# Kernel optimization log

Measured on AMD Instinct MI355X. Metric: run time of the kernel, lower is better.

Reference implementation:

```python
import jax, jax.numpy as jnp
import numpy as np

N_NODES = 59392        # batch_size * node_each_graph = 512 * 116
N_EDGES = 1187840      # avg degree 20

def _graph_conv(h, src, dst, W, b, out_norm, in_norm):
    # DGL GraphConv, norm='both': act((D_in^-1/2 A D_out^-1/2 h) W + b)
    h = h * out_norm[:, None]
    m = jax.ops.segment_sum(h[src], dst, num_segments=N_NODES)  # sparse aggregation
    m = m * in_norm[:, None]
    return jax.nn.relu(m @ W + b)

def setup_inputs() -> dict:
    key = jax.random.key(0)
    ks = jax.random.split(key, 8)
    feat = jax.random.normal(ks[0], (N_NODES, 116), dtype=jnp.float32)
    src = jax.random.randint(ks[1], (N_EDGES,), 0, N_NODES)
    dst = jax.random.randint(ks[2], (N_EDGES,), 0, N_NODES)
    W1 = jax.random.normal(ks[3], (116, 64), dtype=jnp.float32) * 0.05
    b1 = jnp.zeros((64,), dtype=jnp.float32)
    W2 = jax.random.normal(ks[4], (64, 64), dtype=jnp.float32) * 0.05
    b2 = jnp.zeros((64,), dtype=jnp.float32)
    Wc = jax.random.normal(ks[5], (116 * 64, 2), dtype=jnp.float32) * 0.05
    bc = jnp.zeros((2,), dtype=jnp.float32)
    return {"feat": feat, "src": src, "dst": dst, "batch_size": 512,
            "W1": W1, "b1": b1, "W2": W2, "b2": b2, "Wc": Wc, "bc": bc}

def reference(feat, src, dst, batch_size, W1, b1, W2, b2, Wc, bc):
    ones = jnp.ones((N_EDGES,), dtype=jnp.float32)
    out_deg = jax.ops.segment_sum(ones, src, num_segments=N_NODES)
    in_deg = jax.ops.segment_sum(ones, dst, num_segments=N_NODES)
    out_norm = jax.lax.rsqrt(jnp.maximum(out_deg, 1.0))
    in_norm = jax.lax.rsqrt(jnp.maximum(in_deg, 1.0))
    h = _graph_conv(feat, src, dst, W1, b1, out_norm, in_norm)
    # dropout is identity in eval mode
    h = _graph_conv(h, src, dst, W2, b2, out_norm, in_norm)
    h = h.reshape(batch_size, -1)  # (B, node_each_graph * hid)
    return h @ Wc + bc
```

## Files before the change

kernel.cpp:

```cpp
#include <hip/hip_runtime.h>

#define N_NODES 59392
#define N_EDGES 1187840
#define F_IN 116
#define F_HID 64
#define BATCH 512
#define NPG 116
#define CCAP 64
#define NSLD 80
#define EPSD (N_EDGES / NSLD)
#define NSLS 80
#define EPSS (N_EDGES / NSLS)
#define NBIN4 (N_NODES / 4)
#define GPB 4
#define NPB (NPG / GPB)
#define SCAN_BLK (N_NODES / 256)
#define GEMM_BLK 640

typedef __attribute__((ext_vector_type(8))) short short8;
typedef __attribute__((ext_vector_type(4))) float float4v;
typedef __attribute__((ext_vector_type(2))) float float2v;

__device__ __forceinline__ float u2f(unsigned u) {
    union { unsigned u; float f; } x; x.u = u; return x.f;
}
__device__ __forceinline__ float bf2f(unsigned short h) {
    union { unsigned u; float f; } x; x.u = (unsigned)h << 16; return x.f;
}
__device__ __forceinline__ unsigned short f2bf(float f) {
    union { float f; unsigned u; } x; x.f = f;
    unsigned r = x.u + 0x7FFF + ((x.u >> 16) & 1);
    return (unsigned short)(r >> 16);
}

__global__ __launch_bounds__(1024) void hist_kernel(const int* __restrict__ src,
                                                    const int* __restrict__ dst,
                                                    unsigned char* __restrict__ cnt2,
                                                    unsigned char* __restrict__ cnt2s) {
    __shared__ unsigned bins[NBIN4];
    int tid = threadIdx.x;
    int b = blockIdx.x;
    const int* __restrict__ idx;
    unsigned char* outp;
    int slice;
    if (b < NSLD) {
        slice = b; idx = dst; outp = cnt2;
    } else {
        slice = b - NSLD; idx = src; outp = cnt2s;
    }
    long ebase = (long)slice * EPSD;
    for (int k = tid; k < NBIN4; k += 1024) bins[k] = 0;
    __syncthreads();
    for (int k = tid; k < EPSD; k += 1024) {
        int v = idx[ebase + k];
        atomicAdd(&bins[v >> 2], 1u << ((v & 3) * 8));
    }
    __syncthreads();
    unsigned* op = (unsigned*)(outp + (size_t)slice * N_NODES);
    for (int k = tid; k < NBIN4; k += 1024) op[k] = bins[k];
}

__global__ __launch_bounds__(256) void scan_kernel(unsigned char* __restrict__ cnt2,
                                                   const unsigned char* __restrict__ cnt2s,
                                                   float* __restrict__ onorm,
                                                   float* __restrict__ inorm,
                                                   int* __restrict__ ncnt,
                                                   unsigned short* __restrict__ A1h) {
    int d = blockIdx.x * 256 + threadIdx.x;
    int run = 0;
    #pragma unroll 1
    for (int i = 0; i < NSLD; i += 8) {
        int c[8];
        #pragma unroll
        for (int j = 0; j < 8; ++j) c[j] = cnt2[(size_t)(i + j) * N_NODES + d];
        #pragma unroll
        for (int j = 0; j < 8; ++j) {
            cnt2[(size_t)(i + j) * N_NODES + d] = (unsigned char)run;
            run += c[j];
        }
    }
    int o = 0;
    #pragma unroll 1
    for (int i = 0; i < NSLS; i += 8) {
        int c[8];
        #pragma unroll
        for (int j = 0; j < 8; ++j) c[j] = cnt2s[(size_t)(i + j) * N_NODES + d];
        #pragma unroll
        for (int j = 0; j < 8; ++j) o += c[j];
    }
    onorm[d] = rsqrtf(fmaxf((float)o, 1.0f));
    inorm[d] = rsqrtf(fmaxf((float)run, 1.0f));
    ncnt[d] = run < CCAP ? run : CCAP;
    if (blockIdx.x == 0 && threadIdx.x < 16)
        ((unsigned long long*)(A1h + (size_t)N_NODES * F_HID))[threadIdx.x] = 0ull;
}

__global__ __launch_bounds__(256) void gemm_place_kernel(const int* __restrict__ src,
                                                         const int* __restrict__ dst,
                                                         const unsigned char* __restrict__ cnt2,
                                                         unsigned short* __restrict__ ebuf,
                                                         const float* __restrict__ feat,
                                                         const float* __restrict__ W1,
                                                         const float* __restrict__ onorm,
                                                         unsigned short* __restrict__ A1h) {
    __shared__ unsigned cur[NBIN4];
    if (blockIdx.x < NSLD) {
        int tid = threadIdx.x;
        int slice = blockIdx.x;
        long ebase = (long)slice * EPSD;
        const unsigned* pp = (const unsigned*)(cnt2 + (size_t)slice * N_NODES);
        for (int k = tid; k < NBIN4; k += 256) cur[k] = pp[k];
        __syncthreads();
        #pragma unroll 1
        for (int t = 0; t < 14; ++t) {
            int k = t * 1024 + tid;
            int d0 = dst[ebase + k],        s0 = src[ebase + k];
            int d1 = dst[ebase + k + 256],  s1 = src[ebase + k + 256];
            int d2 = dst[ebase + k + 512],  s2 = src[ebase + k + 512];
            int d3 = dst[ebase + k + 768],  s3 = src[ebase + k + 768];
            #define PLACE1(dd, ss)                                                    \
                { int sh = ((dd) & 3) * 8;                                            \
                  unsigned old = atomicAdd(&cur[(dd) >> 2], 1u << sh);                \
                  unsigned pos = (old >> sh) & 0xFFu;                                 \
                  if (pos < CCAP) ebuf[(size_t)(dd) * CCAP + pos] = (unsigned short)(ss); }
            PLACE1(d0, s0) PLACE1(d1, s1) PLACE1(d2, s2) PLACE1(d3, s3)
        }
        {
            int k = 14336 + tid;
            int d0 = dst[ebase + k], s0 = src[ebase + k];
            PLACE1(d0, s0)
            k = 14592 + tid;
            d0 = dst[ebase + k]; s0 = src[ebase + k];
            PLACE1(d0, s0)
            #undef PLACE1
        }
        return;
    }
    int lane = threadIdx.x & 63;
    int c16 = lane & 15, quad = lane >> 4;
    short8 Bhi[4][4], Blo[4][4];
    #pragma unroll
    for (int kiter = 0; kiter < 4; ++kiter) {
        #pragma unroll
        for (int t = 0; t < 4; ++t) {
            #pragma unroll
            for (int j = 0; j < 8; ++j) {
                int k = kiter * 32 + quad * 8 + j;
                float w = (k < F_IN) ? W1[k * F_HID + t * 16 + c16] : 0.f;
                unsigned short hi = f2bf(w);
                unsigned short lo = f2bf(w - bf2f(hi));
                Bhi[kiter][t][j] = (short)hi;
                Blo[kiter][t][j] = (short)lo;
            }
        }
    }
    int bid = blockIdx.x - NSLD;
    int wid = (bid * 256 + threadIdx.x) >> 6;
    int nwaves = (GEMM_BLK * 256) >> 6;
    const int ntiles = N_NODES / 16;
    for (int tile = wid; tile < ntiles; tile += nwaves) {
        int base = tile * 16;
        int row = base + c16;
        float on = onorm[row];
        const float* fp = feat + (size_t)row * F_IN;
        float4v acc[4] = {{0.f,0.f,0.f,0.f},{0.f,0.f,0.f,0.f},{0.f,0.f,0.f,0.f},{0.f,0.f,0.f,0.f}};
        #pragma unroll
        for (int kiter = 0; kiter < 4; ++kiter) {
            int koff = kiter * 32 + quad * 8;
            float f[8];
            if (koff + 8 <= F_IN) {
                float4 x = *(const float4*)(fp + koff);
                float4 y = *(const float4*)(fp + koff + 4);
                f[0]=x.x; f[1]=x.y; f[2]=x.z; f[3]=x.w;
                f[4]=y.x; f[5]=y.y; f[6]=y.z; f[7]=y.w;
            } else {
                #pragma unroll
                for (int j = 0; j < 8; ++j) f[j] = (koff + j < F_IN) ? fp[koff + j] : 0.f;
            }
            short8 ah, al;
            #pragma unroll
            for (int j = 0; j < 8; ++j) {
                float v = f[j] * on;
                unsigned short hi = f2bf(v);
                ah[j] = (short)hi;
                al[j] = (short)f2bf(v - bf2f(hi));
            }
            #pragma unroll
            for (int t = 0; t < 4; ++t) {
                acc[t] = __builtin_amdgcn_mfma_f32_16x16x32_bf16(ah, Bhi[kiter][t], acc[t], 0, 0, 0);
                acc[t] = __builtin_amdgcn_mfma_f32_16x16x32_bf16(al, Bhi[kiter][t], acc[t], 0, 0, 0);
                acc[t] = __builtin_amdgcn_mfma_f32_16x16x32_bf16(ah, Blo[kiter][t], acc[t], 0, 0, 0);
            }
        }
        #pragma unroll
        for (int t = 0; t < 4; ++t) {
            #pragma unroll
            for (int r = 0; r < 4; ++r) {
                int node = base + quad * 4 + r;
                A1h[(size_t)node * F_HID + t * 16 + c16] = f2bf(acc[t][r]);
            }
        }
    }
}

__device__ __forceinline__ void gather2n(const unsigned* __restrict__ base,
                                         const unsigned short* __restrict__ ebuf,
                                         int va, int vb, int na, int nb,
                                         int c16, int g4, int sh16,
                                         float& a0, float& a1, float& a2, float& a3,
                                         float& b0, float& b1, float& b2, float& b3) {
    const unsigned long long* ea = (const unsigned long long*)(ebuf + (size_t)va * CCAP);
    const unsigned long long* eb = (const unsigned long long*)(ebuf + (size_t)vb * CCAP);
    unsigned long long cha[8], chb[8];
    #pragma unroll
    for (int t = 0; t < 8; ++t) cha[t] = __builtin_nontemporal_load(&ea[t]);
    #pragma unroll
    for (int t = 0; t < 8; ++t) chb[t] = __builtin_nontemporal_load(&eb[t]);
    int ida[8], idb[8];
    #pragma unroll
    for (int t = 0; t < 8; ++t) {
        ida[t] = (t * 4 + g4 < na) ? (int)((cha[t] >> sh16) & 0xFFFFu) : N_NODES;
        idb[t] = (t * 4 + g4 < nb) ? (int)((chb[t] >> sh16) & 0xFFFFu) : N_NODES;
    }
    unsigned long long rwa[8], rwb[8];
    #pragma unroll
    for (int t = 0; t < 8; ++t) rwa[t] = *(const unsigned long long*)(base + ida[t] * 32 + c16 * 2);
    #pragma unroll
    for (int t = 0; t < 8; ++t) rwb[t] = *(const unsigned long long*)(base + idb[t] * 32 + c16 * 2);
    float2v A01 = {0.f, 0.f}, A23 = {0.f, 0.f}, B01 = {0.f, 0.f}, B23 = {0.f, 0.f};
    #pragma unroll
    for (int t = 0; t < 8; ++t) {
        unsigned lo = (unsigned)rwa[t], hi = (unsigned)(rwa[t] >> 32);
        float2v x; x.x = u2f(lo << 16); x.y = u2f(lo & 0xFFFF0000u);
        float2v y; y.x = u2f(hi << 16); y.y = u2f(hi & 0xFFFF0000u);
        A01 += x; A23 += y;
    }
    #pragma unroll
    for (int t = 0; t < 8; ++t) {
        unsigned lo = (unsigned)rwb[t], hi = (unsigned)(rwb[t] >> 32);
        float2v x; x.x = u2f(lo << 16); x.y = u2f(lo & 0xFFFF0000u);
        float2v y; y.x = u2f(hi << 16); y.y = u2f(hi & 0xFFFF0000u);
        B01 += x; B23 += y;
    }
    int nqa = (na + 3) >> 2;
    #pragma unroll 1
    for (int t = 8; t < nqa; ++t) {
        unsigned long long c = __builtin_nontemporal_load(&ea[t]);
        int e = t * 4 + g4;
        int ix = (e < na) ? (int)((c >> sh16) & 0xFFFFu) : N_NODES;
        unsigned long long w = *(const unsigned long long*)(base + ix * 32 + c16 * 2);
        unsigned lo = (unsigned)w, hi = (unsigned)(w >> 32);
        float2v x; x.x = u2f(lo << 16); x.y = u2f(lo & 0xFFFF0000u);
        float2v y; y.x = u2f(hi << 16); y.y = u2f(hi & 0xFFFF0000u);
        A01 += x; A23 += y;
    }
    int nqb = (nb + 3) >> 2;
    #pragma unroll 1
    for (int t = 8; t < nqb; ++t) {
        unsigned long long c = __builtin_nontemporal_load(&eb[t]);
        int e = t * 4 + g4;
        int ix = (e < nb) ? (int)((c >> sh16) & 0xFFFFu) : N_NODES;
        unsigned long long w = *(const unsigned long long*)(base + ix * 32 + c16 * 2);
        unsigned lo = (unsigned)w, hi = (unsigned)(w >> 32);
        float2v x; x.x = u2f(lo << 16); x.y = u2f(lo & 0xFFFF0000u);
        float2v y; y.x = u2f(hi << 16); y.y = u2f(hi & 0xFFFF0000u);
        B01 += x; B23 += y;
    }
    a0 = A01.x; a1 = A01.y; a2 = A23.x; a3 = A23.y;
    b0 = B01.x; b1 = B01.y; b2 = B23.x; b3 = B23.y;
    a0 += __shfl_xor(a0, 16); a1 += __shfl_xor(a1, 16);
    a2 += __shfl_xor(a2, 16); a3 += __shfl_xor(a3, 16);
    a0 += __shfl_xor(a0, 32); a1 += __shfl_xor(a1, 32);
    a2 += __shfl_xor(a2, 32); a3 += __shfl_xor(a3, 32);
    b0 += __shfl_xor(b0, 16); b1 += __shfl_xor(b1, 16);
    b2 += __shfl_xor(b2, 16); b3 += __shfl_xor(b3, 16);
    b0 += __shfl_xor(b0, 32); b1 += __shfl_xor(b1, 32);
    b2 += __shfl_xor(b2, 32); b3 += __shfl_xor(b3, 32);
}

__global__ __launch_bounds__(256) void gather1_kernel(const int* __restrict__ ncnt,
                                                      const unsigned short* __restrict__ ebuf,
                                                      const unsigned short* __restrict__ A1h,
                                                      const float* __restrict__ onorm,
                                                      const float* __restrict__ inorm,
                                                      const float* __restrict__ b1,
                                                      unsigned short* __restrict__ H1h,
                                                      float* __restrict__ out) {
    if (blockIdx.x == 0) {
        int t = threadIdx.x;
        for (int k = t; k < BATCH * 2; k += 256) out[k] = 0.f;
        if (t < 16) ((unsigned long long*)(H1h + (size_t)N_NODES * F_HID))[t] = 0ull;
    }
    int lane = threadIdx.x & 63;
    int wu = __builtin_amdgcn_readfirstlane(threadIdx.x >> 6);
    int c16 = lane & 15, g4 = lane >> 4, sh16 = g4 * 16;
    int va = blockIdx.x * 8 + wu * 2;
    int vb = va + 1;
    int na = ncnt[va], nb = ncnt[vb];
    const unsigned* base = (const unsigned*)A1h;
    float4 b1q = ((const float4*)b1)[c16];
    float a0, a1, a2, a3, b0, b1v, b2v, b3;
    gather2n(base, ebuf, va, vb, na, nb, c16, g4, sh16,
             a0, a1, a2, a3, b0, b1v, b2v, b3);
    float ina = inorm[va], ona = onorm[va];
    float inb = inorm[vb], onb = onorm[vb];
    float ha0 = fmaxf(ina * a0 + b1q.x, 0.f) * ona;
    float ha1 = fmaxf(ina * a1 + b1q.y, 0.f) * ona;
    float ha2 = fmaxf(ina * a2 + b1q.z, 0.f) * ona;
    float ha3 = fmaxf(ina * a3 + b1q.w, 0.f) * ona;
    float hb0 = fmaxf(inb * b0 + b1q.x, 0.f) * onb;
    float hb1 = fmaxf(inb * b1v + b1q.y, 0.f) * onb;
    float hb2 = fmaxf(inb * b2v + b1q.z, 0.f) * onb;
    float hb3 = fmaxf(inb * b3 + b1q.w, 0.f) * onb;
    if (g4 == 0) {
        unsigned lo = (unsigned)f2bf(ha0) | ((unsigned)f2bf(ha1) << 16);
        unsigned hi = (unsigned)f2bf(ha2) | ((unsigned)f2bf(ha3) << 16);
        ((unsigned long long*)H1h)[(size_t)va * 16 + c16] = ((unsigned long long)hi << 32) | lo;
        lo = (unsigned)f2bf(hb0) | ((unsigned)f2bf(hb1) << 16);
        hi = (unsigned)f2bf(hb2) | ((unsigned)f2bf(hb3) << 16);
        ((unsigned long long*)H1h)[(size_t)vb * 16 + c16] = ((unsigned long long)hi << 32) | lo;
    }
}

__global__ __launch_bounds__(256) void readout_kernel(const int* __restrict__ ncnt,
                                                      const unsigned short* __restrict__ ebuf,
                                                      const unsigned short* __restrict__ H1h,
                                                      const float* __restrict__ inorm,
                                                      const float* __restrict__ b2,
                                                      const float* __restrict__ W2,
                                                      const float* __restrict__ Wc,
                                                      const float* __restrict__ bc,
                                                      float* __restrict__ out) {
    __shared__ float Gs[NPB][F_HID];
    __shared__ float ls[8];
    int g = blockIdx.x >> 2, part = blockIdx.x & 3;
    int nbase = g * NPG + part * NPB;
    int lane = threadIdx.x & 63;
    int wu = __builtin_amdgcn_readfirstlane(threadIdx.x >> 6);
    int c16 = lane & 15, g4 = lane >> 4, sh16 = g4 * 16;
    const unsigned* base = (const unsigned*)H1h;
    for (int nl = wu * 2; nl + 1 < NPB; nl += 8) {
        int va = nbase + nl, vb = va + 1;
        int na = ncnt[va], nb = ncnt[vb];
        float a0, a1, a2, a3, b0, b1, b2v, b3;
        gather2n(base, ebuf, va, vb, na, nb, c16, g4, sh16,
                 a0, a1, a2, a3, b0, b1, b2v, b3);
        if (g4 == 0) {
            float4 m4; m4.x = a0; m4.y = a1; m4.z = a2; m4.w = a3;
            *(float4*)&Gs[nl][c16 * 4] = m4;
            m4.x = b0; m4.y = b1; m4.z = b2v; m4.w = b3;
            *(float4*)&Gs[nl + 1][c16 * 4] = m4;
        }
    }
    if (wu == 2) {
        int v = nbase + 28;
        int n = ncnt[v];
        float a0, a1, a2, a3, d0, d1, d2, d3;
        gather2n(base, ebuf, v, v, n, 0, c16, g4, sh16,
                 a0, a1, a2, a3, d0, d1, d2, d3);
        if (g4 == 0) {
            float4 m4; m4.x = a0; m4.y = a1; m4.z = a2; m4.w = a3;
            *(float4*)&Gs[28][c16 * 4] = m4;
        }
    }
    __syncthreads();
    float w2[F_HID];
    #pragma unroll
    for (int k = 0; k < F_HID; ++k) w2[k] = W2[k * F_HID + lane];
    float b2l = b2[lane];
    float s0 = 0.f, s1 = 0.f;
    for (int nl = wu; nl < NPB; nl += 4) {
        int v = nbase + nl;
        float acc = 0.f;
        #pragma unroll
        for (int k = 0; k < F_HID; k += 4) {
            float4 gk = *(const float4*)&Gs[nl][k];
            acc += gk.x * w2[k] + gk.y * w2[k + 1] + gk.z * w2[k + 2] + gk.w * w2[k + 3];
        }
        float h = fmaxf(inorm[v] * acc + b2l, 0.f);
        float2 w = ((const float2*)Wc)[(part * NPB + nl) * F_HID + lane];
        s0 += h * w.x;
        s1 += h * w.y;
    }
    #pragma unroll
    for (int off = 32; off > 0; off >>= 1) {
        s0 += __shfl_down(s0, off);
        s1 += __shfl_down(s1, off);
    }
    if (lane == 0) { ls[wu * 2] = s0; ls[wu * 2 + 1] = s1; }
    __syncthreads();
    if (threadIdx.x < 2) {
        float t = 0.f;
        #pragma unroll
        for (int w = 0; w < 4; ++w) t += ls[w * 2 + threadIdx.x];
        if (part == 0) t += bc[threadIdx.x];
        atomicAdd(&out[g * 2 + threadIdx.x], t);
    }
}

extern "C" void kernel_launch(void* const* d_in, const int* in_sizes, int n_in,
                              void* d_out, int out_size, void* d_ws, size_t ws_size,
                              hipStream_t stream) {
    const float* feat = (const float*)d_in[0];
    const int*   src  = (const int*)d_in[1];
    const int*   dst  = (const int*)d_in[2];
    const float* W1 = (const float*)d_in[4];
    const float* b1 = (const float*)d_in[5];
    const float* W2 = (const float*)d_in[6];
    const float* b2 = (const float*)d_in[7];
    const float* Wc = (const float*)d_in[8];
    const float* bc = (const float*)d_in[9];
    float* out = (float*)d_out;

    unsigned char* cnt2  = (unsigned char*)d_ws;
    unsigned char* cnt2s = cnt2 + (size_t)NSLD * N_NODES;
    float* onorm = (float*)(cnt2s + (size_t)NSLS * N_NODES);
    float* inorm = onorm + N_NODES + 1;
    int* ncnt    = (int*)(inorm + N_NODES);
    unsigned short* ebuf = (unsigned short*)(((unsigned long long)(ncnt + N_NODES) + 255ull) & ~255ull);
    unsigned short* A1h  = ebuf + (size_t)N_NODES * CCAP;
    unsigned short* H1h  = (unsigned short*)cnt2;

    hist_kernel<<<NSLD + NSLS, 1024, 0, stream>>>(src, dst, cnt2, cnt2s);
    scan_kernel<<<SCAN_BLK, 256, 0, stream>>>(cnt2, cnt2s, onorm, inorm, ncnt, A1h);
    gemm_place_kernel<<<NSLD + GEMM_BLK, 256, 0, stream>>>(src, dst, cnt2, ebuf,
                                                           feat, W1, onorm, A1h);
    gather1_kernel<<<N_NODES / 8, 256, 0, stream>>>(ncnt, ebuf, A1h, onorm, inorm, b1, H1h, out);
    readout_kernel<<<BATCH * GPB, 256, 0, stream>>>(ncnt, ebuf, H1h, inorm, b2, W2, Wc, bc, out);
}
```

Before: 189.3 us.

## Split fused GEMM/placement kernel and double destination slice count

The combined gemm_place kernel is split into a standalone 1024-thread place_kernel and a separate gemm1_kernel, launched one after the other. The number of destination-edge slices goes from 80 to 160, so histogram and placement run across more blocks, each handling fewer edges. The aim is to fill more CUs during the atomic-heavy binning and placement. In exchange it gives up the concurrent overlap of placement with the GEMM, adds a kernel launch, and makes the scan read twice as many per-slice counters.

```diff
diff --git a/kernel.cpp b/kernel.cpp
--- a/kernel.cpp
+++ b/kernel.cpp
@@ -7,7 +7,7 @@
 #define BATCH 512
 #define NPG 116
 #define CCAP 64
-#define NSLD 80
+#define NSLD 160
 #define EPSD (N_EDGES / NSLD)
 #define NSLS 80
 #define EPSS (N_EDGES / NSLS)
@@ -42,16 +42,16 @@
     int b = blockIdx.x;
     const int* __restrict__ idx;
     unsigned char* outp;
-    int slice;
+    int slice, nedge;
     if (b < NSLD) {
-        slice = b; idx = dst; outp = cnt2;
+        slice = b; idx = dst; outp = cnt2; nedge = EPSD;
     } else {
-        slice = b - NSLD; idx = src; outp = cnt2s;
-    }
-    long ebase = (long)slice * EPSD;
+        slice = b - NSLD; idx = src; outp = cnt2s; nedge = EPSS;
+    }
+    long ebase = (long)slice * nedge;
     for (int k = tid; k < NBIN4; k += 1024) bins[k] = 0;
     __syncthreads();
-    for (int k = tid; k < EPSD; k += 1024) {
+    for (int k = tid; k < nedge; k += 1024) {
         int v = idx[ebase + k];
         atomicAdd(&bins[v >> 2], 1u << ((v & 3) * 8));
     }
@@ -95,47 +95,42 @@
         ((unsigned long long*)(A1h + (size_t)N_NODES * F_HID))[threadIdx.x] = 0ull;
 }
 
-__global__ __launch_bounds__(256) void gemm_place_kernel(const int* __restrict__ src,
-                                                         const int* __restrict__ dst,
-                                                         const unsigned char* __restrict__ cnt2,
-                                                         unsigned short* __restrict__ ebuf,
-                                                         const float* __restrict__ feat,
-                                                         const float* __restrict__ W1,
-                                                         const float* __restrict__ onorm,
-                                                         unsigned short* __restrict__ A1h) {
+__global__ __launch_bounds__(1024) void place_kernel(const int* __restrict__ src,
+                                                     const int* __restrict__ dst,
+                                                     const unsigned char* __restrict__ cnt2,
+                                                     unsigned short* __restrict__ ebuf) {
     __shared__ unsigned cur[NBIN4];
-    if (blockIdx.x < NSLD) {
-        int tid = threadIdx.x;
-        int slice = blockIdx.x;
-        long ebase = (long)slice * EPSD;
-        const unsigned* pp = (const unsigned*)(cnt2 + (size_t)slice * N_NODES);
-        for (int k = tid; k < NBIN4; k += 256) cur[k] = pp[k];
-        __syncthreads();
+    int tid = threadIdx.x;
+    int slice = blockIdx.x;
+    long ebase = (long)slice * EPSD;
+    const unsigned* pp = (const unsigned*)(cnt2 + (size_t)slice * N_NODES);
+    for (int k = tid; k < NBIN4; k += 1024) cur[k] = pp[k];
+    __syncthreads();
+    {
         #pragma unroll 1
-        for (int t = 0; t < 14; ++t) {
+        for (int t = 0; t < 7; ++t) {
             int k = t * 1024 + tid;
-            int d0 = dst[ebase + k],        s0 = src[ebase + k];
-            int d1 = dst[ebase + k + 256],  s1 = src[ebase + k + 256];
-            int d2 = dst[ebase + k + 512],  s2 = src[ebase + k + 512];
-            int d3 = dst[ebase + k + 768],  s3 = src[ebase + k + 768];
-            #define PLACE1(dd, ss)                                                    \
-                { int sh = ((dd) & 3) * 8;                                            \
-                  unsigned old = atomicAdd(&cur[(dd) >> 2], 1u << sh);                \
-                  unsigned pos = (old >> sh) & 0xFFu;                                 \
-                  if (pos < CCAP) ebuf[(size_t)(dd) * CCAP + pos] = (unsigned short)(ss); }
-            PLACE1(d0, s0) PLACE1(d1, s1) PLACE1(d2, s2) PLACE1(d3, s3)
-        }
-        {
-            int k = 14336 + tid;
             int d0 = dst[ebase + k], s0 = src[ebase + k];
-            PLACE1(d0, s0)
-            k = 14592 + tid;
-            d0 = dst[ebase + k]; s0 = src[ebase + k];
-            PLACE1(d0, s0)
-            #undef PLACE1
-        }
-        return;
-    }
+            int sh = (d0 & 3) * 8;
+            unsigned old = atomicAdd(&cur[d0 >> 2], 1u << sh);
+            unsigned pos = (old >> sh) & 0xFFu;
+            if (pos < CCAP) ebuf[(size_t)d0 * CCAP + pos] = (unsigned short)s0;
+        }
+        if (tid < 256) {
+            int k = 7168 + tid;
+            int d0 = dst[ebase + k], s0 = src[ebase + k];
+            int sh = (d0 & 3) * 8;
+            unsigned old = atomicAdd(&cur[d0 >> 2], 1u << sh);
+            unsigned pos = (old >> sh) & 0xFFu;
+            if (pos < CCAP) ebuf[(size_t)d0 * CCAP + pos] = (unsigned short)s0;
+        }
+    }
+}
+
+__global__ __launch_bounds__(256) void gemm1_kernel(const float* __restrict__ feat,
+                                                    const float* __restrict__ W1,
+                                                    const float* __restrict__ onorm,
+                                                    unsigned short* __restrict__ A1h) {
     int lane = threadIdx.x & 63;
     int c16 = lane & 15, quad = lane >> 4;
     short8 Bhi[4][4], Blo[4][4];
@@ -154,8 +149,7 @@
             }
         }
     }
-    int bid = blockIdx.x - NSLD;
-    int wid = (bid * 256 + threadIdx.x) >> 6;
+    int wid = (blockIdx.x * 256 + threadIdx.x) >> 6;
     int nwaves = (GEMM_BLK * 256) >> 6;
     const int ntiles = N_NODES / 16;
     for (int tile = wid; tile < ntiles; tile += nwaves) {
@@ -423,8 +417,8 @@
 
     hist_kernel<<<NSLD + NSLS, 1024, 0, stream>>>(src, dst, cnt2, cnt2s);
     scan_kernel<<<SCAN_BLK, 256, 0, stream>>>(cnt2, cnt2s, onorm, inorm, ncnt, A1h);
-    gemm_place_kernel<<<NSLD + GEMM_BLK, 256, 0, stream>>>(src, dst, cnt2, ebuf,
-                                                           feat, W1, onorm, A1h);
+    place_kernel<<<NSLD, 1024, 0, stream>>>(src, dst, cnt2, ebuf);
+    gemm1_kernel<<<GEMM_BLK, 256, 0, stream>>>(feat, W1, onorm, A1h);
     gather1_kernel<<<N_NODES / 8, 256, 0, stream>>>(ncnt, ebuf, A1h, onorm, inorm, b1, H1h, out);
     readout_kernel<<<BATCH * GPB, 256, 0, stream>>>(ncnt, ebuf, H1h, inorm, b2, W2, Wc, bc, out);
 }
```

Result: slower. 199.6 us (+5.4%).
